# Kernel optimization log

Measured on AMD Instinct MI355X. Metric: run time of the kernel, lower is better.

Reference implementation:

```python
import jax, jax.numpy as jnp
import numpy as np

H = 1024
NH = 16
HD = H // NH

def setup_inputs() -> dict:
    key = jax.random.key(0)
    ks = jax.random.split(key, 8)
    s = 1.0 / np.sqrt(H)
    hidden_states = jax.random.normal(ks[0], (2, 2048, H), dtype=jnp.float32)
    attention_mask = jnp.zeros((2, 1, 1, 2048), dtype=jnp.float32)
    Wq = jax.random.uniform(ks[1], (H, H), jnp.float32, -s, s)
    bq = jax.random.uniform(ks[2], (H,), jnp.float32, -s, s)
    Wk = jax.random.uniform(ks[3], (H, H), jnp.float32, -s, s)
    bk = jax.random.uniform(ks[4], (H,), jnp.float32, -s, s)
    Wv = jax.random.uniform(ks[5], (H, H), jnp.float32, -s, s)
    bv = jax.random.uniform(ks[6], (H,), jnp.float32, -s, s)
    return {"hidden_states": hidden_states, "attention_mask": attention_mask,
            "Wq": Wq, "bq": bq, "Wk": Wk, "bk": bk, "Wv": Wv, "bv": bv}

def _split_heads(x):
    B, L, _ = x.shape
    return x.reshape(B, L, NH, HD).transpose(0, 2, 1, 3)  # [B, nh, L, hd]

def reference(hidden_states, attention_mask, Wq, bq, Wk, bk, Wv, bv):
    # QKV projections (nn.Linear: x @ W.T + b)
    Q = _split_heads(hidden_states @ Wq.T + bq)
    K = _split_heads(hidden_states @ Wk.T + bk)
    V = _split_heads(hidden_states @ Wv.T + bv)
    scale = 1.0 / np.sqrt(HD)
    scores = jnp.einsum('bhqd,bhkd->bhqk', Q, K) * scale  # [B, nh, L, L]
    scores = scores + attention_mask
    probs = jax.nn.softmax(scores, axis=-1)  # dropout in eval mode = identity
    context = jnp.einsum('bhqk,bhkd->bhqd', probs, V)
    B, _, L, _ = context.shape
    return context.transpose(0, 2, 1, 3).reshape(B, L, H)
```

## Files before the change

kernel.cpp:

```cpp
#include <hip/hip_runtime.h>
#include <math.h>
#include <stdint.h>

#define H_DIM 1024
#define NH 16
#define HD 64
#define B_DIM 2
#define L_DIM 2048
#define M_TOT (B_DIM * L_DIM)

typedef __bf16 bf16_t;
typedef __bf16 bf16x8 __attribute__((ext_vector_type(8)));
typedef __bf16 bf16x4 __attribute__((ext_vector_type(4)));
typedef float  f32x4  __attribute__((ext_vector_type(4)));

#define AS1 const __attribute__((address_space(1))) void*
#define AS3 __attribute__((address_space(3))) void*

__global__ __launch_bounds__(256)
void cast_all(const float* __restrict__ x,
              const float* __restrict__ Wq, const float* __restrict__ Wk,
              const float* __restrict__ Wv, bf16_t* __restrict__ dst)
{
    const size_t idx = ((size_t)blockIdx.x * 256 + threadIdx.x) * 4;
    const float* src;
    size_t off;
    if (idx < (size_t)M_TOT * H_DIM) { src = x; off = idx; }
    else {
        size_t j = idx - (size_t)M_TOT * H_DIM;
        int z = (int)(j >> 20);
        off = j & ((1u << 20) - 1);
        src = (z == 0) ? Wq : (z == 1) ? Wk : Wv;
    }
    const float4 v = *(const float4*)(src + off);
    bf16x4 o;
    o[0] = (bf16_t)v.x; o[1] = (bf16_t)v.y;
    o[2] = (bf16_t)v.z; o[3] = (bf16_t)v.w;
    *(bf16x4*)(dst + idx) = o;
}

__global__ __launch_bounds__(256)
void qkv_mfma(const bf16_t* __restrict__ xb, const bf16_t* __restrict__ wb,
              const float* __restrict__ bq, const float* __restrict__ bk,
              const float* __restrict__ bv,
              bf16_t* __restrict__ qb, bf16_t* __restrict__ kb,
              bf16_t* __restrict__ vt)
{
    __shared__ bf16_t As0[128 * 32];
    __shared__ bf16_t Bs0[128 * 32];
    __shared__ bf16_t As1[128 * 32];
    __shared__ bf16_t Bs1[128 * 32];

    const int tid  = threadIdx.x;
    const int z    = blockIdx.z;
    const int bm   = blockIdx.x * 128;
    const int bn   = blockIdx.y * 128;
    const bf16_t* W    = wb + (size_t)z * H_DIM * H_DIM;
    const float*  bias = (z == 0) ? bq : (z == 1) ? bk : bv;

    const int wave = tid >> 6;
    const int lane = tid & 63;
    const int lc   = lane & 15;
    const int quad = lane >> 4;
    const int wm   = wave >> 1;
    const int wn   = wave & 1;

    f32x4 acc[4][4];
    #pragma unroll
    for (int i = 0; i < 4; ++i)
        #pragma unroll
        for (int j = 0; j < 4; ++j)
            acc[i][j] = (f32x4){0.f, 0.f, 0.f, 0.f};

    const int srow = tid >> 2;
    const int sseg = tid & 3;
    const bf16_t* gA = xb + (size_t)(bm + srow) * H_DIM + (sseg ^ (srow & 3)) * 8;
    const bf16_t* gB = W  + (size_t)(bn + srow) * H_DIM + (sseg ^ (srow & 3)) * 8;
    const int woff = wave * 1024;

    auto stage = [&](int k0, bf16_t* A_, bf16_t* B_) {
        __builtin_amdgcn_global_load_lds((AS1)(gA + k0),
            (AS3)((char*)A_ + woff), 16, 0, 0);
        __builtin_amdgcn_global_load_lds((AS1)(gA + k0 + (size_t)64 * H_DIM),
            (AS3)((char*)A_ + woff + 4096), 16, 0, 0);
        __builtin_amdgcn_global_load_lds((AS1)(gB + k0),
            (AS3)((char*)B_ + woff), 16, 0, 0);
        __builtin_amdgcn_global_load_lds((AS1)(gB + k0 + (size_t)64 * H_DIM),
            (AS3)((char*)B_ + woff + 4096), 16, 0, 0);
    };

    const int slot = (quad ^ (lc & 3)) * 8;
    auto compute = [&](const bf16_t* A_, const bf16_t* B_) {
        bf16x8 a[4], b[4];
        #pragma unroll
        for (int mi = 0; mi < 4; ++mi)
            a[mi] = *(const bf16x8*)(A_ + (wm * 64 + mi * 16 + lc) * 32 + slot);
        #pragma unroll
        for (int ni = 0; ni < 4; ++ni)
            b[ni] = *(const bf16x8*)(B_ + (wn * 64 + ni * 16 + lc) * 32 + slot);
        #pragma unroll
        for (int mi = 0; mi < 4; ++mi)
            #pragma unroll
            for (int ni = 0; ni < 4; ++ni)
                acc[mi][ni] = __builtin_amdgcn_mfma_f32_16x16x32_bf16(
                    a[mi], b[ni], acc[mi][ni], 0, 0, 0);
    };

    stage(0, As0, Bs0);
    #pragma unroll 1
    for (int kk = 0; kk < 16; ++kk) {
        const int k0 = kk * 64;
        __syncthreads();
        stage(k0 + 32, As1, Bs1);
        compute(As0, Bs0);
        __syncthreads();
        if (k0 + 64 < H_DIM) stage(k0 + 64, As0, Bs0);
        compute(As1, Bs1);
    }

    const int nb = bn + wn * 64;
    float biasv[4];
    #pragma unroll
    for (int ni = 0; ni < 4; ++ni) biasv[ni] = bias[nb + ni * 16 + lc];

    #pragma unroll
    for (int mi = 0; mi < 4; ++mi) {
        const int m0 = bm + wm * 64 + mi * 16 + quad * 4;
        if (z == 2) {
            const int b_ = m0 >> 11;
            const int l0 = m0 & 2047;
            #pragma unroll
            for (int ni = 0; ni < 4; ++ni) {
                const int n = nb + ni * 16 + lc;
                const int h = n >> 6, d = n & 63;
                bf16x4 pk;
                #pragma unroll
                for (int r = 0; r < 4; ++r)
                    pk[r] = (bf16_t)(acc[mi][ni][r] + biasv[ni]);
                *(bf16x4*)(vt + (((size_t)(b_ * NH + h)) * HD + d) * L_DIM + l0) = pk;
            }
        } else {
            bf16_t* dst = (z == 0) ? qb : kb;
            #pragma unroll
            for (int r = 0; r < 4; ++r) {
                const int m  = m0 + r;
                const int b_ = m >> 11;
                const int l  = m & 2047;
                #pragma unroll
                for (int ni = 0; ni < 4; ++ni) {
                    const int n = nb + ni * 16 + lc;
                    const int h = n >> 6, d = n & 63;
                    dst[(((size_t)(b_ * NH + h)) * L_DIM + l) * HD + d] =
                        (bf16_t)(acc[mi][ni][r] + biasv[ni]);
                }
            }
        }
    }
}

#define EXP_C   0.180336879f
#define LOG2E   1.442695041f
#define EXP_SH  11.541560327f

__device__ __forceinline__ void attn_tile32(
    int kbase, bool pre,
    const bf16_t* curK, const bf16_t* curV,
    bf16_t* nxtK, bf16_t* nxtV,
    const bf16_t* gK, const bf16_t* gV,
    bf16_t* Ps, const float* mrow, int lc, int quad,
    const bf16x8 (&bQ)[2][2], f32x4 (&o)[2][4], float (&rs)[2])
{
    __builtin_amdgcn_s_waitcnt(0x0F70);

    const int e = lc & 7;

    bf16x8 kf[2][2];
    #pragma unroll
    for (int ni = 0; ni < 2; ++ni) {
        const bf16_t* p = curK + (ni * 16 + lc) * 64;
        kf[ni][0] = *(const bf16x8*)(p + ((quad ^ e) << 3));
        kf[ni][1] = *(const bf16x8*)(p + (((quad ^ e) ^ 4) << 3));
    }

    if (pre) {
        const int nk = kbase + 32;
        #pragma unroll
        for (int i = 0; i < 4; ++i) {
            __builtin_amdgcn_global_load_lds(
                (AS1)(gK + (size_t)nk * 64 + i * 512),
                (AS3)(nxtK + i * 512), 16, 0, 0);
            __builtin_amdgcn_global_load_lds(
                (AS1)(gV + nk + i * 32768),
                (AS3)(nxtV + i * 512), 16, 0, 0);
        }
    }

    float mvs[2][4];
    #pragma unroll
    for (int ni = 0; ni < 2; ++ni) {
        const float4 mv = *(const float4*)(mrow + kbase + ni * 16 + quad * 4);
        mvs[ni][0] = mv.x * LOG2E - EXP_SH;
        mvs[ni][1] = mv.y * LOG2E - EXP_SH;
        mvs[ni][2] = mv.z * LOG2E - EXP_SH;
        mvs[ni][3] = mv.w * LOG2E - EXP_SH;
    }

    #pragma unroll
    for (int f = 0; f < 2; ++f) {
        f32x4 s[2];
        #pragma unroll
        for (int ni = 0; ni < 2; ++ni) {
            f32x4 t = (f32x4){0.f, 0.f, 0.f, 0.f};
            t = __builtin_amdgcn_mfma_f32_16x16x32_bf16(kf[ni][0], bQ[f][0], t, 0, 0, 0);
            t = __builtin_amdgcn_mfma_f32_16x16x32_bf16(kf[ni][1], bQ[f][1], t, 0, 0, 0);
            s[ni] = t;
        }
        float acc = 0.f;
        #pragma unroll
        for (int ni = 0; ni < 2; ++ni) {
            bf16x4 pk;
            #pragma unroll
            for (int r = 0; r < 4; ++r) {
                const float p = __builtin_amdgcn_exp2f(s[ni][r] * EXP_C + mvs[ni][r]);
                acc += p;
                pk[r] = (bf16_t)p;
            }
            const int c = f * 4 + ni * 2 + (quad >> 1);
            *(bf16x4*)(Ps + lc * 64 + ((c ^ e) << 3) + ((quad & 1) << 2)) = pk;
        }
        rs[f] += acc;
    }

    bf16x8 vf[4];
    const int e2 = lc >> 1;
    #pragma unroll
    for (int dg = 0; dg < 4; ++dg) {
        const int p  = dg * 8 + (lc >> 1);
        const int ch = (((lc & 1) << 2) + quad) ^ e2;
        vf[dg] = *(const bf16x8*)(curV + p * 64 + (ch << 3));
    }

    #pragma unroll
    for (int f = 0; f < 2; ++f) {
        const int c = f * 4 + quad;
        const bf16x8 bP = *(const bf16x8*)(Ps + lc * 64 + ((c ^ e) << 3));
        #pragma unroll
        for (int dg = 0; dg < 4; ++dg)
            o[f][dg] = __builtin_amdgcn_mfma_f32_16x16x32_bf16(vf[dg], bP, o[f][dg], 0, 0, 0);
    }
}

__global__ __launch_bounds__(64, 2)
void attn_mfma(const bf16_t* __restrict__ qb, const bf16_t* __restrict__ kb,
               const bf16_t* __restrict__ vt, const float* __restrict__ mask,
               float* __restrict__ out)
{
    __shared__ bf16_t Ks0[32 * 64];
    __shared__ bf16_t Ks1[32 * 64];
    __shared__ bf16_t Vs0[32 * 64];
    __shared__ bf16_t Vs1[32 * 64];
    __shared__ bf16_t Ps[16 * 64];

    const int lane = threadIdx.x & 63;
    const int lc   = lane & 15;
    const int quad = lane >> 4;
    const int rl   = lane >> 3;
    const int sg   = lane & 7;

    const int n    = blockIdx.x;
    const int bh   = (n & 7) * 4 + ((n >> 3) & 3);
    const int q0   = (n >> 5) * 32;
    const int b_   = bh >> 4;
    const int h    = bh & 15;

    bf16x8 bQ[2][2];
    #pragma unroll
    for (int f = 0; f < 2; ++f) {
        const bf16_t* Qp = qb + ((size_t)bh * L_DIM + q0 + f * 16 + lc) * HD + quad * 8;
        bQ[f][0] = *(const bf16x8*)(Qp);
        bQ[f][1] = *(const bf16x8*)(Qp + 32);
    }

    const bf16_t* Kbase = kb + (size_t)bh * L_DIM * HD;
    const bf16_t* Vbase = vt + (size_t)bh * HD * L_DIM;
    const float*  mrow  = mask + (size_t)b_ * L_DIM;

    const bf16_t* gK = Kbase + rl * 64 + (sg ^ rl) * 8;
    const int cV = sg ^ rl;
    const bf16_t* gV = Vbase + (size_t)(rl * 2 + (cV >> 2)) * L_DIM + (cV & 3) * 8;

    f32x4 o[2][4];
    #pragma unroll
    for (int f = 0; f < 2; ++f)
        #pragma unroll
        for (int dg = 0; dg < 4; ++dg) o[f][dg] = (f32x4){0.f, 0.f, 0.f, 0.f};
    float rs[2] = {0.f, 0.f};

    #pragma unroll
    for (int i = 0; i < 4; ++i) {
        __builtin_amdgcn_global_load_lds(
            (AS1)(gK + i * 512),
            (AS3)(Ks0 + i * 512), 16, 0, 0);
        __builtin_amdgcn_global_load_lds(
            (AS1)(gV + i * 32768),
            (AS3)(Vs0 + i * 512), 16, 0, 0);
    }

    #pragma unroll 1
    for (int t2 = 0; t2 < 32; ++t2) {
        const int kb0 = t2 * 64;
        attn_tile32(kb0,      true,     Ks0, Vs0, Ks1, Vs1, gK, gV, Ps,
                    mrow, lc, quad, bQ, o, rs);
        attn_tile32(kb0 + 32, t2 < 31,  Ks1, Vs1, Ks0, Vs0, gK, gV, Ps,
                    mrow, lc, quad, bQ, o, rs);
    }

    #pragma unroll
    for (int f = 0; f < 2; ++f) {
        float l = rs[f];
        l += __shfl_xor(l, 16);
        l += __shfl_xor(l, 32);
        const float inv = 1.0f / l;
        float* orow = out + ((size_t)(b_ * L_DIM + q0 + f * 16 + lc)) * H_DIM
                    + h * HD + quad * 4;
        #pragma unroll
        for (int dg = 0; dg < 4; ++dg) {
            f32x4 w = o[f][dg];
            w[0] *= inv; w[1] *= inv; w[2] *= inv; w[3] *= inv;
            *(f32x4*)(orow + dg * 16) = w;
        }
    }
}

extern "C" void kernel_launch(void* const* d_in, const int* in_sizes, int n_in,
                              void* d_out, int out_size, void* d_ws, size_t ws_size,
                              hipStream_t stream) {
    const float* hidden = (const float*)d_in[0];
    const float* mask   = (const float*)d_in[1];
    const float* Wq     = (const float*)d_in[2];
    const float* bq     = (const float*)d_in[3];
    const float* Wk     = (const float*)d_in[4];
    const float* bk     = (const float*)d_in[5];
    const float* Wv     = (const float*)d_in[6];
    const float* bv     = (const float*)d_in[7];
    float* out = (float*)d_out;

    const size_t XN = (size_t)M_TOT * H_DIM;
    const size_t WN = (size_t)3 * H_DIM * H_DIM;
    bf16_t* xwb = (bf16_t*)d_ws;
    bf16_t* qb  = xwb + XN + WN;
    bf16_t* kb  = qb + XN;
    bf16_t* vt  = kb + XN;

    cast_all<<<(int)((XN + WN) / 1024), 256, 0, stream>>>(hidden, Wq, Wk, Wv, xwb);

    dim3 g1(M_TOT / 128, H_DIM / 128, 3);
    qkv_mfma<<<g1, 256, 0, stream>>>(xwb, xwb + XN, bq, bk, bv, qb, kb, vt);

    attn_mfma<<<2048, 64, 0, stream>>>(qb, kb, vt, mask, out);
}
```

Before: 182.7 us.

## Load V fragments directly from global and remap QKV GEMM block order

```diff
diff --git a/kernel.cpp b/kernel.cpp
--- a/kernel.cpp
+++ b/kernel.cpp
@@ -52,9 +52,14 @@
     __shared__ bf16_t Bs1[128 * 32];
 
     const int tid  = threadIdx.x;
-    const int z    = blockIdx.z;
-    const int bm   = blockIdx.x * 128;
-    const int bn   = blockIdx.y * 128;
+
+    const int n    = blockIdx.x;
+    const int i    = n >> 3;
+    const int bm   = (i / 3) * 128;
+    const int bnz  = (n & 7) * 3 + (i % 3);
+    const int bn   = (bnz & 7) * 128;
+    const int z    = bnz >> 3;
+
     const bf16_t* W    = wb + (size_t)z * H_DIM * H_DIM;
     const float*  bias = (z == 0) ? bq : (z == 1) ? bk : bv;
 
@@ -67,10 +72,10 @@
 
     f32x4 acc[4][4];
     #pragma unroll
-    for (int i = 0; i < 4; ++i)
+    for (int ii = 0; ii < 4; ++ii)
         #pragma unroll
         for (int j = 0; j < 4; ++j)
-            acc[i][j] = (f32x4){0.f, 0.f, 0.f, 0.f};
+            acc[ii][j] = (f32x4){0.f, 0.f, 0.f, 0.f};
 
     const int srow = tid >> 2;
     const int sseg = tid & 3;
@@ -131,8 +136,8 @@
             const int l0 = m0 & 2047;
             #pragma unroll
             for (int ni = 0; ni < 4; ++ni) {
-                const int n = nb + ni * 16 + lc;
-                const int h = n >> 6, d = n & 63;
+                const int nn = nb + ni * 16 + lc;
+                const int h = nn >> 6, d = nn & 63;
                 bf16x4 pk;
                 #pragma unroll
                 for (int r = 0; r < 4; ++r)
@@ -148,8 +153,8 @@
                 const int l  = m & 2047;
                 #pragma unroll
                 for (int ni = 0; ni < 4; ++ni) {
-                    const int n = nb + ni * 16 + lc;
-                    const int h = n >> 6, d = n & 63;
+                    const int nn = nb + ni * 16 + lc;
+                    const int h = nn >> 6, d = nn & 63;
                     dst[(((size_t)(b_ * NH + h)) * L_DIM + l) * HD + d] =
                         (bf16_t)(acc[mi][ni][r] + biasv[ni]);
                 }
@@ -164,9 +169,8 @@
 
 __device__ __forceinline__ void attn_tile32(
     int kbase, bool pre,
-    const bf16_t* curK, const bf16_t* curV,
-    bf16_t* nxtK, bf16_t* nxtV,
-    const bf16_t* gK, const bf16_t* gV,
+    const bf16_t* curK, bf16_t* nxtK,
+    const bf16_t* gK, const bf16_t* Vbase,
     bf16_t* Ps, const float* mrow, int lc, int quad,
     const bf16x8 (&bQ)[2][2], f32x4 (&o)[2][4], float (&rs)[2])
 {
@@ -174,6 +178,12 @@
 
     const int e = lc & 7;
 
+    bf16x8 vf[4];
+    #pragma unroll
+    for (int dg = 0; dg < 4; ++dg)
+        vf[dg] = *(const bf16x8*)(Vbase + (size_t)(dg * 16 + lc) * L_DIM
+                                  + kbase + quad * 8);
+
     bf16x8 kf[2][2];
     #pragma unroll
     for (int ni = 0; ni < 2; ++ni) {
@@ -185,14 +195,10 @@
     if (pre) {
         const int nk = kbase + 32;
         #pragma unroll
-        for (int i = 0; i < 4; ++i) {
+        for (int i = 0; i < 4; ++i)
             __builtin_amdgcn_global_load_lds(
                 (AS1)(gK + (size_t)nk * 64 + i * 512),
                 (AS3)(nxtK + i * 512), 16, 0, 0);
-            __builtin_amdgcn_global_load_lds(
-                (AS1)(gV + nk + i * 32768),
-                (AS3)(nxtV + i * 512), 16, 0, 0);
-        }
     }
 
     float mvs[2][4];
@@ -231,15 +237,6 @@
         rs[f] += acc;
     }
 
-    bf16x8 vf[4];
-    const int e2 = lc >> 1;
-    #pragma unroll
-    for (int dg = 0; dg < 4; ++dg) {
-        const int p  = dg * 8 + (lc >> 1);
-        const int ch = (((lc & 1) << 2) + quad) ^ e2;
-        vf[dg] = *(const bf16x8*)(curV + p * 64 + (ch << 3));
-    }
-
     #pragma unroll
     for (int f = 0; f < 2; ++f) {
         const int c = f * 4 + quad;
@@ -257,8 +254,6 @@
 {
     __shared__ bf16_t Ks0[32 * 64];
     __shared__ bf16_t Ks1[32 * 64];
-    __shared__ bf16_t Vs0[32 * 64];
-    __shared__ bf16_t Vs1[32 * 64];
     __shared__ bf16_t Ps[16 * 64];
 
     const int lane = threadIdx.x & 63;
@@ -286,8 +281,6 @@
     const float*  mrow  = mask + (size_t)b_ * L_DIM;
 
     const bf16_t* gK = Kbase + rl * 64 + (sg ^ rl) * 8;
-    const int cV = sg ^ rl;
-    const bf16_t* gV = Vbase + (size_t)(rl * 2 + (cV >> 2)) * L_DIM + (cV & 3) * 8;
 
     f32x4 o[2][4];
     #pragma unroll
@@ -297,21 +290,17 @@
     float rs[2] = {0.f, 0.f};
 
     #pragma unroll
-    for (int i = 0; i < 4; ++i) {
+    for (int i = 0; i < 4; ++i)
         __builtin_amdgcn_global_load_lds(
             (AS1)(gK + i * 512),
             (AS3)(Ks0 + i * 512), 16, 0, 0);
-        __builtin_amdgcn_global_load_lds(
-            (AS1)(gV + i * 32768),
-            (AS3)(Vs0 + i * 512), 16, 0, 0);
-    }
 
     #pragma unroll 1
     for (int t2 = 0; t2 < 32; ++t2) {
         const int kb0 = t2 * 64;
-        attn_tile32(kb0,      true,     Ks0, Vs0, Ks1, Vs1, gK, gV, Ps,
+        attn_tile32(kb0,      true,     Ks0, Ks1, gK, Vbase, Ps,
                     mrow, lc, quad, bQ, o, rs);
-        attn_tile32(kb0 + 32, t2 < 31,  Ks1, Vs1, Ks0, Vs0, gK, gV, Ps,
+        attn_tile32(kb0 + 32, t2 < 31,  Ks1, Ks0, gK, Vbase, Ps,
                     mrow, lc, quad, bQ, o, rs);
     }
 
@@ -354,8 +343,7 @@
 
     cast_all<<<(int)((XN + WN) / 1024), 256, 0, stream>>>(hidden, Wq, Wk, Wv, xwb);
 
-    dim3 g1(M_TOT / 128, H_DIM / 128, 3);
-    qkv_mfma<<<g1, 256, 0, stream>>>(xwb, xwb + XN, bq, bk, bv, qb, kb, vt);
+    qkv_mfma<<<768, 256, 0, stream>>>(xwb, xwb + XN, bq, bk, bv, qb, kb, vt);
 
     attn_mfma<<<2048, 64, 0, stream>>>(qb, kb, vt, mask, out);
 }
```

New measurement: 212.4 us. +16.3%, slower.

## Fuse Q/K/V projections into one block sharing the A tile with triple buffering

Applied to the files above, without the earlier changes.

```diff
diff --git a/kernel.cpp b/kernel.cpp
--- a/kernel.cpp
+++ b/kernel.cpp
@@ -39,7 +39,7 @@
     *(bf16x4*)(dst + idx) = o;
 }
 
-__global__ __launch_bounds__(256)
+__global__ __launch_bounds__(256, 1)
 void qkv_mfma(const bf16_t* __restrict__ xb, const bf16_t* __restrict__ wb,
               const float* __restrict__ bq, const float* __restrict__ bk,
               const float* __restrict__ bv,
@@ -47,16 +47,16 @@
               bf16_t* __restrict__ vt)
 {
     __shared__ bf16_t As0[128 * 32];
-    __shared__ bf16_t Bs0[128 * 32];
     __shared__ bf16_t As1[128 * 32];
-    __shared__ bf16_t Bs1[128 * 32];
-
-    const int tid  = threadIdx.x;
-    const int z    = blockIdx.z;
-    const int bm   = blockIdx.x * 128;
-    const int bn   = blockIdx.y * 128;
-    const bf16_t* W    = wb + (size_t)z * H_DIM * H_DIM;
-    const float*  bias = (z == 0) ? bq : (z == 1) ? bk : bv;
+    __shared__ bf16_t As2[128 * 32];
+    __shared__ bf16_t Bs0[3][128 * 32];
+    __shared__ bf16_t Bs1[3][128 * 32];
+    __shared__ bf16_t Bs2[3][128 * 32];
+
+    const int tid = threadIdx.x;
+    const int n   = blockIdx.x;
+    const int bn  = (n & 7) * 128;
+    const int bm  = (n >> 3) * 128;
 
     const int wave = tid >> 6;
     const int lane = tid & 63;
@@ -65,93 +65,117 @@
     const int wm   = wave >> 1;
     const int wn   = wave & 1;
 
-    f32x4 acc[4][4];
-    #pragma unroll
-    for (int i = 0; i < 4; ++i)
-        #pragma unroll
-        for (int j = 0; j < 4; ++j)
-            acc[i][j] = (f32x4){0.f, 0.f, 0.f, 0.f};
+    f32x4 acc[3][4][4];
+    #pragma unroll
+    for (int z = 0; z < 3; ++z)
+        #pragma unroll
+        for (int i = 0; i < 4; ++i)
+            #pragma unroll
+            for (int j = 0; j < 4; ++j)
+                acc[z][i][j] = (f32x4){0.f, 0.f, 0.f, 0.f};
 
     const int srow = tid >> 2;
     const int sseg = tid & 3;
     const bf16_t* gA = xb + (size_t)(bm + srow) * H_DIM + (sseg ^ (srow & 3)) * 8;
-    const bf16_t* gB = W  + (size_t)(bn + srow) * H_DIM + (sseg ^ (srow & 3)) * 8;
+    const bf16_t* gB = wb + (size_t)(bn + srow) * H_DIM + (sseg ^ (srow & 3)) * 8;
     const int woff = wave * 1024;
 
-    auto stage = [&](int k0, bf16_t* A_, bf16_t* B_) {
+    auto stage = [&](int k0, bf16_t* A_, bf16_t (*B_)[128 * 32]) {
         __builtin_amdgcn_global_load_lds((AS1)(gA + k0),
             (AS3)((char*)A_ + woff), 16, 0, 0);
         __builtin_amdgcn_global_load_lds((AS1)(gA + k0 + (size_t)64 * H_DIM),
             (AS3)((char*)A_ + woff + 4096), 16, 0, 0);
-        __builtin_amdgcn_global_load_lds((AS1)(gB + k0),
-            (AS3)((char*)B_ + woff), 16, 0, 0);
-        __builtin_amdgcn_global_load_lds((AS1)(gB + k0 + (size_t)64 * H_DIM),
-            (AS3)((char*)B_ + woff + 4096), 16, 0, 0);
+        #pragma unroll
+        for (int z = 0; z < 3; ++z) {
+            const bf16_t* g = gB + (size_t)z * H_DIM * H_DIM + k0;
+            __builtin_amdgcn_global_load_lds((AS1)(g),
+                (AS3)((char*)B_[z] + woff), 16, 0, 0);
+            __builtin_amdgcn_global_load_lds((AS1)(g + (size_t)64 * H_DIM),
+                (AS3)((char*)B_[z] + woff + 4096), 16, 0, 0);
+        }
     };
 
     const int slot = (quad ^ (lc & 3)) * 8;
-    auto compute = [&](const bf16_t* A_, const bf16_t* B_) {
-        bf16x8 a[4], b[4];
+    auto compute = [&](const bf16_t* A_, const bf16_t (*B_)[128 * 32]) {
+        bf16x8 a[4];
         #pragma unroll
         for (int mi = 0; mi < 4; ++mi)
             a[mi] = *(const bf16x8*)(A_ + (wm * 64 + mi * 16 + lc) * 32 + slot);
         #pragma unroll
-        for (int ni = 0; ni < 4; ++ni)
-            b[ni] = *(const bf16x8*)(B_ + (wn * 64 + ni * 16 + lc) * 32 + slot);
-        #pragma unroll
-        for (int mi = 0; mi < 4; ++mi)
+        for (int z = 0; z < 3; ++z) {
+            bf16x8 b[4];
             #pragma unroll
             for (int ni = 0; ni < 4; ++ni)
-                acc[mi][ni] = __builtin_amdgcn_mfma_f32_16x16x32_bf16(
-                    a[mi], b[ni], acc[mi][ni], 0, 0, 0);
+                b[ni] = *(const bf16x8*)(B_[z] + (wn * 64 + ni * 16 + lc) * 32 + slot);
+            #pragma unroll
+            for (int mi = 0; mi < 4; ++mi)
+                #pragma unroll
+                for (int ni = 0; ni < 4; ++ni)
+                    acc[z][mi][ni] = __builtin_amdgcn_mfma_f32_16x16x32_bf16(
+                        a[mi], b[ni], acc[z][mi][ni], 0, 0, 0);
+        }
     };
 
-    stage(0, As0, Bs0);
+    auto step = [&](int kk, bf16_t* cA, bf16_t (*cB)[128 * 32],
+                    bf16_t* nA, bf16_t (*nB)[128 * 32], bool doStage) {
+        __builtin_amdgcn_s_waitcnt(0x0F78);
+        __builtin_amdgcn_s_barrier();
+        if (doStage) stage((kk + 2) * 32, nA, nB);
+        compute(cA, cB);
+    };
+
+    stage(0,  As0, Bs0);
+    stage(32, As1, Bs1);
     #pragma unroll 1
-    for (int kk = 0; kk < 16; ++kk) {
-        const int k0 = kk * 64;
-        __syncthreads();
-        stage(k0 + 32, As1, Bs1);
-        compute(As0, Bs0);
-        __syncthreads();
-        if (k0 + 64 < H_DIM) stage(k0 + 64, As0, Bs0);
-        compute(As1, Bs1);
-    }
+    for (int t = 0; t < 10; ++t) {
+        const int kk = t * 3;
+        step(kk,     As0, Bs0, As2, Bs2, true);
+        step(kk + 1, As1, Bs1, As0, Bs0, true);
+        step(kk + 2, As2, Bs2, As1, Bs1, true);
+    }
+    step(30, As0, Bs0, As2, Bs2, false);
+    __builtin_amdgcn_s_waitcnt(0x0F70);
+    __builtin_amdgcn_s_barrier();
+    compute(As1, Bs1);
 
     const int nb = bn + wn * 64;
-    float biasv[4];
-    #pragma unroll
-    for (int ni = 0; ni < 4; ++ni) biasv[ni] = bias[nb + ni * 16 + lc];
-
-    #pragma unroll
-    for (int mi = 0; mi < 4; ++mi) {
-        const int m0 = bm + wm * 64 + mi * 16 + quad * 4;
-        if (z == 2) {
-            const int b_ = m0 >> 11;
-            const int l0 = m0 & 2047;
-            #pragma unroll
-            for (int ni = 0; ni < 4; ++ni) {
-                const int n = nb + ni * 16 + lc;
-                const int h = n >> 6, d = n & 63;
-                bf16x4 pk;
-                #pragma unroll
-                for (int r = 0; r < 4; ++r)
-                    pk[r] = (bf16_t)(acc[mi][ni][r] + biasv[ni]);
-                *(bf16x4*)(vt + (((size_t)(b_ * NH + h)) * HD + d) * L_DIM + l0) = pk;
-            }
-        } else {
-            bf16_t* dst = (z == 0) ? qb : kb;
-            #pragma unroll
-            for (int r = 0; r < 4; ++r) {
-                const int m  = m0 + r;
-                const int b_ = m >> 11;
-                const int l  = m & 2047;
+    #pragma unroll
+    for (int z = 0; z < 3; ++z) {
+        const float* bias = (z == 0) ? bq : (z == 1) ? bk : bv;
+        float biasv[4];
+        #pragma unroll
+        for (int ni = 0; ni < 4; ++ni) biasv[ni] = bias[nb + ni * 16 + lc];
+
+        #pragma unroll
+        for (int mi = 0; mi < 4; ++mi) {
+            const int m0 = bm + wm * 64 + mi * 16 + quad * 4;
+            if (z == 2) {
+                const int b_ = m0 >> 11;
+                const int l0 = m0 & 2047;
                 #pragma unroll
                 for (int ni = 0; ni < 4; ++ni) {
-                    const int n = nb + ni * 16 + lc;
-                    const int h = n >> 6, d = n & 63;
-                    dst[(((size_t)(b_ * NH + h)) * L_DIM + l) * HD + d] =
-                        (bf16_t)(acc[mi][ni][r] + biasv[ni]);
+                    const int nn = nb + ni * 16 + lc;
+                    const int h = nn >> 6, d = nn & 63;
+                    bf16x4 pk;
+                    #pragma unroll
+                    for (int r = 0; r < 4; ++r)
+                        pk[r] = (bf16_t)(acc[z][mi][ni][r] + biasv[ni]);
+                    *(bf16x4*)(vt + (((size_t)(b_ * NH + h)) * HD + d) * L_DIM + l0) = pk;
+                }
+            } else {
+                bf16_t* dst = (z == 0) ? qb : kb;
+                #pragma unroll
+                for (int r = 0; r < 4; ++r) {
+                    const int m  = m0 + r;
+                    const int b_ = m >> 11;
+                    const int l  = m & 2047;
+                    #pragma unroll
+                    for (int ni = 0; ni < 4; ++ni) {
+                        const int nn = nb + ni * 16 + lc;
+                        const int h = nn >> 6, d = nn & 63;
+                        dst[(((size_t)(b_ * NH + h)) * L_DIM + l) * HD + d] =
+                            (bf16_t)(acc[z][mi][ni][r] + biasv[ni]);
+                    }
                 }
             }
         }
@@ -354,8 +378,7 @@
 
     cast_all<<<(int)((XN + WN) / 1024), 256, 0, stream>>>(hidden, Wq, Wk, Wv, xwb);
 
-    dim3 g1(M_TOT / 128, H_DIM / 128, 3);
-    qkv_mfma<<<g1, 256, 0, stream>>>(xwb, xwb + XN, bq, bk, bv, qb, kb, vt);
+    qkv_mfma<<<256, 256, 0, stream>>>(xwb, xwb + XN, bq, bk, bv, qb, kb, vt);
 
     attn_mfma<<<2048, 64, 0, stream>>>(qb, kb, vt, mask, out);
 }
```

Result: no change. 181.3 us (-0.8%).
